# Kernel tuning notes

Measured on AMD Instinct MI355X. Metric: run time of the kernel, lower is better.

Reference implementation:

```python
import jax, jax.numpy as jnp
import numpy as np

N = 50000      # nodes
E = 800000     # edges
IN = 128       # in_dim
OUT = 64       # out_dim
NEG_SLOPE = 0.01  # F.leaky_relu default


def setup_inputs() -> dict:
    key = jax.random.key(0)
    k1, k2, k3, k4, k5 = jax.random.split(key, 5)
    h = jax.random.normal(k1, (N, IN), dtype=jnp.float32)
    # xavier-normal-ish scale for the two linear layers
    W_fc = jax.random.normal(k2, (OUT, IN), dtype=jnp.float32) * (2.0 / (IN + OUT)) ** 0.5
    W_attn = jax.random.normal(k3, (2 * OUT,), dtype=jnp.float32) * (2.0 / (2 * OUT + 1)) ** 0.5
    src = jax.random.randint(k4, (E,), 0, N)
    dst = jax.random.randint(k5, (E,), 0, N)
    return {"h": h, "W_fc": W_fc, "W_attn": W_attn, "src": src, "dst": dst}


def reference(h, W_fc, W_attn, src, dst):
    # z = fc(h): [N, OUT]
    z = jnp.einsum("ni,oi->no", h, W_fc)
    d = z.shape[-1]
    # per-edge attention logit: attn_fc(cat([z_src, z_dst])) == z_src@a_l + z_dst@a_r
    a_l, a_r = W_attn[:d], W_attn[d:]
    zs = z[src]                                   # [E, OUT] gather
    e = jax.nn.leaky_relu(zs @ a_l + z[dst] @ a_r, negative_slope=NEG_SLOPE)  # [E]
    # segment softmax over incoming edges of each dst node
    m = jax.ops.segment_max(e, dst, num_segments=N)          # [N]
    ex = jnp.exp(e - m[dst])                                  # [E]
    denom = jax.ops.segment_sum(ex, dst, num_segments=N)      # [N]
    alpha = ex / denom[dst]                                    # [E]
    # weighted scatter-sum of source features
    out = jax.ops.segment_sum(alpha[:, None] * zs, dst, num_segments=N)  # [N, OUT]
    return out
```

## Files before the change

kernel.cpp:

```cpp
#include <hip/hip_runtime.h>
#include <hip/hip_bf16.h>
#include <math.h>

#define IN_DIM 128
#define OUT_DIM 64
#define NEG_SLOPE 0.01f
#define BCAP 2048
#define EPT 16

typedef __attribute__((ext_vector_type(8))) short bf8_t;
typedef __attribute__((ext_vector_type(4))) float f4_t;

__device__ __forceinline__ bf8_t pack8(float4 a, float4 b) {
    union { bf8_t v; __hip_bfloat162 h[4]; } u;
    u.h[0] = __float22bfloat162_rn(make_float2(a.x, a.y));
    u.h[1] = __float22bfloat162_rn(make_float2(a.z, a.w));
    u.h[2] = __float22bfloat162_rn(make_float2(b.x, b.y));
    u.h[3] = __float22bfloat162_rn(make_float2(b.z, b.w));
    return u.v;
}

__global__ __launch_bounds__(256) void k_front(
    const int* __restrict__ src, const int* __restrict__ dst,
    int* __restrict__ bucket_cursor, unsigned* __restrict__ tmp, int E,
    const float4* __restrict__ h4, const float4* __restrict__ W4,
    const float* __restrict__ Wattn,
    __hip_bfloat16* __restrict__ zb, float* __restrict__ s_l, float* __restrict__ s_r,
    int N, int NP1)
{
    __shared__ int cnt[1024];
    __shared__ int cur[1024];

    if (blockIdx.x < NP1) {
        const int t = threadIdx.x;
        const int base_e = blockIdx.x * (256 * EPT);

        for (int b = t; b < 1024; b += 256) cnt[b] = 0;
        __syncthreads();

        unsigned pArr[EPT];
        #pragma unroll
        for (int i = 0; i < EPT; i++) {
            int ei = base_e + i * 256 + t;
            if (ei < E) {
                int s = src[ei], d = dst[ei];
                int b = d >> 6;
                pArr[i] = ((unsigned)b << 22) | ((unsigned)s << 6) | (unsigned)(d & 63);
                atomicAdd(&cnt[b], 1);
            } else {
                pArr[i] = 0xFFFFFFFFu;
            }
        }
        __syncthreads();

        for (int b = t; b < 1024; b += 256)
            if (cnt[b] > 0)
                cur[b] = atomicAdd(&bucket_cursor[b], cnt[b]);
        __syncthreads();

        #pragma unroll
        for (int i = 0; i < EPT; i++) {
            unsigned p = pArr[i];
            if (p == 0xFFFFFFFFu) continue;
            int b = p >> 22;
            int slot = atomicAdd(&cur[b], 1);
            if (slot < BCAP)
                tmp[(size_t)b * BCAP + slot] = p;
        }
    } else {
        const int lane = threadIdx.x & 63;
        const int wv   = threadIdx.x >> 6;
        const int col  = lane & 15, quad = lane >> 4;
        const int n0   = (blockIdx.x - NP1) * 64 + wv * 16;
        if (n0 >= N) return;

        bf8_t bf[4][4];
        #pragma unroll
        for (int ns = 0; ns < 4; ns++) {
            const float4* wrow = W4 + (size_t)(ns * 16 + col) * (IN_DIM / 4);
            #pragma unroll
            for (int kb = 0; kb < 4; kb++) {
                float4 x = wrow[kb * 8 + quad * 2];
                float4 y = wrow[kb * 8 + quad * 2 + 1];
                bf[kb][ns] = pack8(x, y);
            }
        }

        const int  na = n0 + col;
        const bool nv = (na < N);
        const float4* hrow = h4 + (size_t)(nv ? na : 0) * (IN_DIM / 4);
        const float4 zero = make_float4(0.f, 0.f, 0.f, 0.f);

        f4_t acc[4];
        #pragma unroll
        for (int ns = 0; ns < 4; ns++) acc[ns] = (f4_t){0.f, 0.f, 0.f, 0.f};

        #pragma unroll
        for (int kb = 0; kb < 4; kb++) {
            float4 x = nv ? hrow[kb * 8 + quad * 2]     : zero;
            float4 y = nv ? hrow[kb * 8 + quad * 2 + 1] : zero;
            bf8_t a = pack8(x, y);
            #pragma unroll
            for (int ns = 0; ns < 4; ns++)
                acc[ns] = __builtin_amdgcn_mfma_f32_16x16x32_bf16(a, bf[kb][ns], acc[ns], 0, 0, 0);
        }

        float alv[4], arv[4];
        #pragma unroll
        for (int ns = 0; ns < 4; ns++) {
            alv[ns] = Wattn[ns * 16 + col];
            arv[ns] = Wattn[OUT_DIM + ns * 16 + col];
        }
        #pragma unroll
        for (int r = 0; r < 4; r++) {
            const int nn = n0 + quad * 4 + r;
            float pl = acc[0][r] * alv[0] + acc[1][r] * alv[1] + acc[2][r] * alv[2] + acc[3][r] * alv[3];
            float pr = acc[0][r] * arv[0] + acc[1][r] * arv[1] + acc[2][r] * arv[2] + acc[3][r] * arv[3];
            #pragma unroll
            for (int o = 1; o < 16; o <<= 1) {
                pl += __shfl_xor(pl, o, 64);
                pr += __shfl_xor(pr, o, 64);
            }
            if (nn < N) {
                __hip_bfloat16* zr = zb + (size_t)nn * OUT_DIM;
                #pragma unroll
                for (int ns = 0; ns < 4; ns++)
                    zr[ns * 16 + col] = __float2bfloat16(acc[ns][r]);
                if (col == 0) { s_l[nn] = pl; s_r[nn] = pr; }
            }
        }
    }
}

__global__ __launch_bounds__(256) void k_tail(
    const unsigned* __restrict__ tmp, const int* __restrict__ bucket_cnt,
    const float* __restrict__ s_l, const float* __restrict__ s_r,
    const uint2* __restrict__ zb2, float4* __restrict__ out4, int N)
{
    __shared__ unsigned short sedge[BCAP];
    __shared__ int cnt_s[64], off_s[64], cur_s[64];
    __shared__ float srs[64];

    const int b = blockIdx.x, t = threadIdx.x;
    const int lane = t & 63, wv = t >> 6;
    const int nbase = b * 64;
    int mb = bucket_cnt[b];
    if (mb > BCAP) mb = BCAP;

    if (t < 64) {
        cnt_s[t] = 0;
        int n = nbase + t;
        srs[t] = (n < N) ? s_r[n] : 0.f;
    }
    __syncthreads();

    const unsigned* mybuf = tmp + (size_t)b * BCAP;
    unsigned pl[BCAP / 256];
    int ne = 0;
    for (int i = t; i < mb; i += 256) {
        unsigned p = mybuf[i];
        pl[ne++] = p;
        atomicAdd(&cnt_s[p & 63u], 1);
    }
    __syncthreads();

    if (t < 64) {
        int c = cnt_s[t];
        int inc = c;
        #pragma unroll
        for (int o = 1; o < 64; o <<= 1) {
            int v = __shfl_up(inc, o, 64);
            if (lane >= o) inc += v;
        }
        off_s[t] = inc - c;
        cur_s[t] = inc - c;
    }
    __syncthreads();

    for (int i = 0; i < ne; i++) {
        unsigned p = pl[i];
        int d = p & 63u;
        int slot = atomicAdd(&cur_s[d], 1);
        sedge[slot] = (unsigned short)((p >> 6) & 0xFFFFu);
    }
    __syncthreads();

    const int c4 = lane & 15;
    const int g  = lane >> 4;
    const float4 zero = make_float4(0.f, 0.f, 0.f, 0.f);

    for (int nl = wv; nl < 64; nl += 4) {
        const int n = nbase + nl;
        if (n >= N) continue;
        const int beg = off_s[nl];
        const int deg = cnt_s[nl] - beg;
        const int deg2 = cur_s[nl] - beg;
        const int end = beg + deg2;
        float4* op = out4 + (size_t)n * 16;

        if (deg2 <= 0) {
            if (lane < 16) op[lane] = zero;
            continue;
        }

        const float sr = srs[nl];
        float4 acc = zero;
        float dsum = 0.f;

        for (int cs = beg; cs < end; cs += 64) {
            int i = cs + lane;
            int s_my = 0; float ex_my = 0.f;
            if (i < end) {
                s_my = sedge[i];
                float e = s_l[s_my] + sr;
                e = (e > 0.f) ? e : NEG_SLOPE * e;
                ex_my = __expf(e);
            }
            dsum += ex_my;
            int c = end - cs; if (c > 64) c = 64;
            for (int j = 0; j < c; j += 4) {
                int jj = j + g;
                int   s  = __shfl(s_my, jj & 63, 64);
                float ex = __shfl(ex_my, jj & 63, 64);
                if (jj >= c) ex = 0.f;
                union { uint2 u; __hip_bfloat162 h[2]; } zu;
                zu.u = zb2[(size_t)s * 16 + c4];
                float2 f0 = __bfloat1622float2(zu.h[0]);
                float2 f1 = __bfloat1622float2(zu.h[1]);
                acc.x += ex * f0.x; acc.y += ex * f0.y;
                acc.z += ex * f1.x; acc.w += ex * f1.y;
            }
        }

        #pragma unroll
        for (int off = 16; off <= 32; off <<= 1) {
            acc.x += __shfl_xor(acc.x, off, 64);
            acc.y += __shfl_xor(acc.y, off, 64);
            acc.z += __shfl_xor(acc.z, off, 64);
            acc.w += __shfl_xor(acc.w, off, 64);
        }
        #pragma unroll
        for (int off = 32; off; off >>= 1) dsum += __shfl_xor(dsum, off, 64);

        if (lane < 16) {
            float inv = 1.f / dsum;
            op[c4] = make_float4(acc.x * inv, acc.y * inv, acc.z * inv, acc.w * inv);
        }
    }
}

extern "C" void kernel_launch(void* const* d_in, const int* in_sizes, int n_in,
                              void* d_out, int out_size, void* d_ws, size_t ws_size,
                              hipStream_t stream)
{
    const float* h     = (const float*)d_in[0];
    const float* Wfc   = (const float*)d_in[1];
    const float* Wattn = (const float*)d_in[2];
    const int*   src   = (const int*)d_in[3];
    const int*   dst   = (const int*)d_in[4];
    const int N = in_sizes[0] / IN_DIM;
    const int E = in_sizes[3];
    const int NBK = (N + 63) / 64;
    const int NP1 = (E + 256 * EPT - 1) / (256 * EPT);

    __hip_bfloat16* zb = (__hip_bfloat16*)d_ws;
    float* s_l     = (float*)(zb + (size_t)N * OUT_DIM);
    float* s_r     = s_l + N;
    int*   bcursor = (int*)(s_r + N);
    unsigned* tmp  = (unsigned*)(bcursor + 1024);

    const int nblk_g = (N + 63) / 64;

    hipMemsetAsync(bcursor, 0, 1024 * sizeof(int), stream);

    k_front<<<NP1 + nblk_g, 256, 0, stream>>>(src, dst, bcursor, tmp, E,
                                              (const float4*)h, (const float4*)Wfc, Wattn,
                                              zb, s_l, s_r, N, NP1);
    k_tail <<<NBK, 256, 0, stream>>>(tmp, bcursor, s_l, s_r,
                                     (const uint2*)zb, (float4*)d_out, N);
}
```

Baseline: 156.9 us.

## Precompute edge exp weights in LDS and gather with 8-lane groups per node

Moves the leaky-relu/exp computation into the scatter phase, storing per-edge exp values in shared memory and accumulating the softmax denominator with LDS atomics. The aggregation loop now gives each destination node an 8-thread group that loads 16-byte bf16 chunks, replacing the wave-per-node scheme with its shuffles and cross-lane reductions. This raises the number of nodes processed concurrently and widens the loads. In exchange it adds 8KB of LDS, uses float atomics on the denominator, and leaves per-node loops serial, so high-degree nodes may cause load imbalance within a wave.

After: 142.9 us. -8.9%, faster.

```diff
diff --git a/kernel.cpp b/kernel.cpp
--- a/kernel.cpp
+++ b/kernel.cpp
@@ -135,20 +135,22 @@
 __global__ __launch_bounds__(256) void k_tail(
     const unsigned* __restrict__ tmp, const int* __restrict__ bucket_cnt,
     const float* __restrict__ s_l, const float* __restrict__ s_r,
-    const uint2* __restrict__ zb2, float4* __restrict__ out4, int N)
+    const uint4* __restrict__ zb4, float4* __restrict__ out4, int N)
 {
     __shared__ unsigned short sedge[BCAP];
+    __shared__ float sex[BCAP];
     __shared__ int cnt_s[64], off_s[64], cur_s[64];
-    __shared__ float srs[64];
+    __shared__ float den_s[64], srs[64];
 
     const int b = blockIdx.x, t = threadIdx.x;
-    const int lane = t & 63, wv = t >> 6;
+    const int lane = t & 63;
     const int nbase = b * 64;
     int mb = bucket_cnt[b];
     if (mb > BCAP) mb = BCAP;
 
     if (t < 64) {
         cnt_s[t] = 0;
+        den_s[t] = 0.f;
         int n = nbase + t;
         srs[t] = (n < N) ? s_r[n] : 0.f;
     }
@@ -180,72 +182,55 @@
     for (int i = 0; i < ne; i++) {
         unsigned p = pl[i];
         int d = p & 63u;
+        int s = (p >> 6) & 0xFFFFu;
+        float e = s_l[s] + srs[d];
+        e = (e > 0.f) ? e : NEG_SLOPE * e;
+        float ex = __expf(e);
         int slot = atomicAdd(&cur_s[d], 1);
-        sedge[slot] = (unsigned short)((p >> 6) & 0xFFFFu);
-    }
-    __syncthreads();
-
-    const int c4 = lane & 15;
-    const int g  = lane >> 4;
-    const float4 zero = make_float4(0.f, 0.f, 0.f, 0.f);
-
-    for (int nl = wv; nl < 64; nl += 4) {
+        sedge[slot] = (unsigned short)s;
+        sex[slot]   = ex;
+        atomicAdd(&den_s[d], ex);
+    }
+    __syncthreads();
+
+    const int ch8 = t & 7;
+    const int grp = t >> 3;
+
+    for (int nl = grp; nl < 64; nl += 32) {
         const int n = nbase + nl;
         if (n >= N) continue;
         const int beg = off_s[nl];
-        const int deg = cnt_s[nl] - beg;
-        const int deg2 = cur_s[nl] - beg;
-        const int end = beg + deg2;
-        float4* op = out4 + (size_t)n * 16;
-
-        if (deg2 <= 0) {
-            if (lane < 16) op[lane] = zero;
+        const int end = cur_s[nl];
+        float4* op = out4 + (size_t)n * 16 + ch8 * 2;
+
+        if (end <= beg) {
+            op[0] = make_float4(0.f, 0.f, 0.f, 0.f);
+            op[1] = make_float4(0.f, 0.f, 0.f, 0.f);
             continue;
         }
 
-        const float sr = srs[nl];
-        float4 acc = zero;
-        float dsum = 0.f;
-
-        for (int cs = beg; cs < end; cs += 64) {
-            int i = cs + lane;
-            int s_my = 0; float ex_my = 0.f;
-            if (i < end) {
-                s_my = sedge[i];
-                float e = s_l[s_my] + sr;
-                e = (e > 0.f) ? e : NEG_SLOPE * e;
-                ex_my = __expf(e);
-            }
-            dsum += ex_my;
-            int c = end - cs; if (c > 64) c = 64;
-            for (int j = 0; j < c; j += 4) {
-                int jj = j + g;
-                int   s  = __shfl(s_my, jj & 63, 64);
-                float ex = __shfl(ex_my, jj & 63, 64);
-                if (jj >= c) ex = 0.f;
-                union { uint2 u; __hip_bfloat162 h[2]; } zu;
-                zu.u = zb2[(size_t)s * 16 + c4];
-                float2 f0 = __bfloat1622float2(zu.h[0]);
-                float2 f1 = __bfloat1622float2(zu.h[1]);
-                acc.x += ex * f0.x; acc.y += ex * f0.y;
-                acc.z += ex * f1.x; acc.w += ex * f1.y;
-            }
-        }
-
-        #pragma unroll
-        for (int off = 16; off <= 32; off <<= 1) {
-            acc.x += __shfl_xor(acc.x, off, 64);
-            acc.y += __shfl_xor(acc.y, off, 64);
-            acc.z += __shfl_xor(acc.z, off, 64);
-            acc.w += __shfl_xor(acc.w, off, 64);
-        }
-        #pragma unroll
-        for (int off = 32; off; off >>= 1) dsum += __shfl_xor(dsum, off, 64);
-
-        if (lane < 16) {
-            float inv = 1.f / dsum;
-            op[c4] = make_float4(acc.x * inv, acc.y * inv, acc.z * inv, acc.w * inv);
-        }
+        float a0 = 0.f, a1 = 0.f, a2 = 0.f, a3 = 0.f;
+        float a4 = 0.f, a5 = 0.f, a6 = 0.f, a7 = 0.f;
+
+        for (int i = beg; i < end; ++i) {
+            int   s  = sedge[i];
+            float ex = sex[i];
+            uint4 zv = zb4[(size_t)s * 8 + ch8];
+            float f0 = __uint_as_float(zv.x << 16);
+            float f1 = __uint_as_float(zv.x & 0xffff0000u);
+            float f2 = __uint_as_float(zv.y << 16);
+            float f3 = __uint_as_float(zv.y & 0xffff0000u);
+            float f4 = __uint_as_float(zv.z << 16);
+            float f5 = __uint_as_float(zv.z & 0xffff0000u);
+            float f6 = __uint_as_float(zv.w << 16);
+            float f7 = __uint_as_float(zv.w & 0xffff0000u);
+            a0 += ex * f0; a1 += ex * f1; a2 += ex * f2; a3 += ex * f3;
+            a4 += ex * f4; a5 += ex * f5; a6 += ex * f6; a7 += ex * f7;
+        }
+
+        float inv = 1.f / den_s[nl];
+        op[0] = make_float4(a0 * inv, a1 * inv, a2 * inv, a3 * inv);
+        op[1] = make_float4(a4 * inv, a5 * inv, a6 * inv, a7 * inv);
     }
 }
 
@@ -277,5 +262,5 @@
                                               (const float4*)h, (const float4*)Wfc, Wattn,
                                               zb, s_l, s_r, N, NP1);
     k_tail <<<NBK, 256, 0, stream>>>(tmp, bcursor, s_l, s_r,
-                                     (const uint2*)zb, (float4*)d_out, N);
-}
+                                     (const uint4*)zb, (float4*)d_out, N);
+}
```
